# Kernel optimization log

Hardware: AMD Instinct MI355X
Metric: run time of the kernel (lower is better)

Reference implementation:

```python
import jax, jax.numpy as jnp
import numpy as np

EMB, HID, OUT = 512, 512, 512

def setup_inputs() -> dict:
    key = jax.random.key(0)
    ks = jax.random.split(key, 7)
    s = 1.0 / np.sqrt(EMB + HID)
    so = 1.0 / np.sqrt(2 * HID)
    return {
        "input_seq": jax.random.normal(ks[0], (32, 512, EMB), dtype=jnp.float32),
        "W_f": jax.random.uniform(ks[1], (EMB + HID, HID), jnp.float32, -s, s),
        "b_f": jax.random.uniform(ks[2], (HID,), jnp.float32, -s, s),
        "W_b": jax.random.uniform(ks[3], (EMB + HID, HID), jnp.float32, -s, s),
        "b_b": jax.random.uniform(ks[4], (HID,), jnp.float32, -s, s),
        "W_o": jax.random.uniform(ks[5], (2 * HID, OUT), jnp.float32, -so, so),
        "b_o": jax.random.uniform(ks[6], (OUT,), jnp.float32, -so, so),
    }

def _rnn_scan(xs, W, b, h0, reverse):
    # split W into input and hidden parts to avoid per-step concat
    Wx, Wh = W[:EMB], W[EMB:]
    def step(h, x_t):
        h_new = jnp.tanh(x_t @ Wx + h @ Wh + b)
        return h_new, h_new
    _, hs = jax.lax.scan(step, h0, xs, reverse=reverse)  # hs: [S, B, H]
    return hs

def reference(input_seq, W_f, b_f, W_b, b_b, W_o, b_o):
    B = input_seq.shape[0]
    xs = jnp.swapaxes(input_seq, 0, 1)  # [S, B, E]
    h0 = jnp.zeros((B, HID), input_seq.dtype)
    hs_f = _rnn_scan(xs, W_f, b_f, h0, reverse=False)   # [S, B, H]
    hs_b = _rnn_scan(xs, W_b, b_b, h0, reverse=True)    # [S, B, H], already time-aligned
    bi = jnp.concatenate([hs_f, hs_b], axis=-1)          # [S, B, 2H]
    out = bi @ W_o + b_o                                 # [S, B, O]
    return jnp.swapaxes(out, 0, 1)                       # [B, S, O]
```

## Files before the change

### kernel.cpp

```cpp
#include <hip/hip_runtime.h>
#include <hip/hip_fp16.h>
#include <stdint.h>

#define SEQ 512
#define HIDN 512

typedef _Float16 h2_t __attribute__((ext_vector_type(2)));
typedef _Float16 h8_t __attribute__((ext_vector_type(8)));
typedef float f4_t __attribute__((ext_vector_type(4)));

__device__ __forceinline__ float fdot2f(uint32_t a, uint32_t b, float c) {
#if __has_builtin(__builtin_amdgcn_fdot2)
  return __builtin_amdgcn_fdot2(__builtin_bit_cast(h2_t, a),
                                __builtin_bit_cast(h2_t, b), c, false);
#else
  h2_t ah = __builtin_bit_cast(h2_t, a);
  h2_t bh = __builtin_bit_cast(h2_t, b);
  return c + (float)ah.x * (float)bh.x + (float)ah.y * (float)bh.y;
#endif
}

__global__ void k_cvt(const float4* __restrict__ src, __half2* __restrict__ dst, int n4) {
  int i = blockIdx.x * blockDim.x + threadIdx.x;
  if (i < n4) {
    float4 v = src[i];
    dst[2 * i]     = __floats2half2_rn(v.x, v.y);
    dst[2 * i + 1] = __floats2half2_rn(v.z, v.w);
  }
}

__global__ void k_transpose_cvt(const float* __restrict__ src, __half* __restrict__ dst,
                                int R, int C) {
  __shared__ float tile[32][33];
  int tx = threadIdx.x, ty = threadIdx.y;
  int c0 = blockIdx.x * 32, r0 = blockIdx.y * 32;
#pragma unroll
  for (int i = 0; i < 4; ++i)
    tile[ty + i * 8][tx] = src[(size_t)(r0 + ty + i * 8) * C + c0 + tx];
  __syncthreads();
#pragma unroll
  for (int i = 0; i < 4; ++i)
    dst[(size_t)(c0 + ty + i * 8) * R + r0 + tx] = __float2half(tile[tx][ty + i * 8]);
}

__global__ __launch_bounds__(256, 2) void k_gemm(
    const __half* __restrict__ A, const __half* __restrict__ Bt,
    const float* __restrict__ bias, float* __restrict__ C,
    int M, int N, int K) {
  __shared__ __align__(16) __half As[128 * 32];
  __shared__ __align__(16) __half Bs[128 * 32];
  const int tid = threadIdx.x;
  const int m0 = blockIdx.x * 128;
  const int n0 = blockIdx.y * 128;
  const int w = tid >> 6;
  const int lane = tid & 63;
  const int wm = (w >> 1) * 64;
  const int wn = (w & 1) * 64;
  const int fr = lane & 15;
  const int q = lane >> 4;
  const int lr = tid >> 2;
  const int lc = tid & 3;
  f4_t acc[4][4];
#pragma unroll
  for (int i = 0; i < 4; ++i)
#pragma unroll
    for (int jj = 0; jj < 4; ++jj) acc[i][jj] = (f4_t)(0.f);

  for (int kk = 0; kk < K; kk += 32) {
    *(uint4*)&As[lr * 32 + lc * 8]        = *(const uint4*)&A[(size_t)(m0 + lr) * K + kk + lc * 8];
    *(uint4*)&As[(64 + lr) * 32 + lc * 8] = *(const uint4*)&A[(size_t)(m0 + 64 + lr) * K + kk + lc * 8];
    *(uint4*)&Bs[lr * 32 + lc * 8]        = *(const uint4*)&Bt[(size_t)(n0 + lr) * K + kk + lc * 8];
    *(uint4*)&Bs[(64 + lr) * 32 + lc * 8] = *(const uint4*)&Bt[(size_t)(n0 + 64 + lr) * K + kk + lc * 8];
    __syncthreads();
    h8_t af[4], bf[4];
#pragma unroll
    for (int i = 0; i < 4; ++i) {
      af[i] = *(const h8_t*)&As[(wm + i * 16 + fr) * 32 + q * 8];
      bf[i] = *(const h8_t*)&Bs[(wn + i * 16 + fr) * 32 + q * 8];
    }
#pragma unroll
    for (int i = 0; i < 4; ++i)
#pragma unroll
      for (int jj = 0; jj < 4; ++jj)
        acc[i][jj] = __builtin_amdgcn_mfma_f32_16x16x32_f16(af[i], bf[jj], acc[i][jj], 0, 0, 0);
    __syncthreads();
  }
#pragma unroll
  for (int i = 0; i < 4; ++i) {
    const int row0 = m0 + wm + i * 16 + q * 4;
#pragma unroll
    for (int jj = 0; jj < 4; ++jj) {
      const int col = n0 + wn + jj * 16 + fr;
      const float bv = bias[col];
#pragma unroll
      for (int r = 0; r < 4; ++r)
        C[(size_t)(row0 + r) * N + col] = acc[i][jj][r] + bv;
    }
  }
}

__global__ __launch_bounds__(1024) void k_rnn(
    const __half* __restrict__ WhT_f, const __half* __restrict__ WhT_b,
    const float* __restrict__ A_f, const float* __restrict__ A_b,
    __half* __restrict__ bi) {
  __shared__ __align__(16) uint4 ldsw4[9 * 1024];
  __shared__ __align__(16) __half hbuf[2][HIDN];
  __shared__ float psum[2][HIDN];
  const int t = threadIdx.x;
  const int j = t & 511;
  const int half = t >> 9;
  const int d = blockIdx.x & 1;
  const int b = blockIdx.x >> 1;
  const __half* WhT = d ? WhT_b : WhT_f;
  const float* A = (d ? A_b : A_f) + (size_t)b * SEQ * HIDN;
  __half* birow = bi + (size_t)b * SEQ * 1024 + d * HIDN + j;

  const uint4* wrow4 = (const uint4*)(WhT + (size_t)j * HIDN);
  uint4 wv[23];
#pragma unroll
  for (int i = 0; i < 23; ++i) wv[i] = wrow4[half * 32 + i];
#pragma unroll
  for (int p = 0; p < 9; ++p) ldsw4[p * 1024 + t] = wrow4[half * 32 + 23 + p];
  if (half == 0) hbuf[0][j] = __float2half(0.f);
  __syncthreads();

  const int tstep = d ? -1 : 1;
  int tt = d ? (SEQ - 1) : 0;
  float a_next = A[(size_t)tt * HIDN + j];
  int cur = 0;
  for (int s = 0; s < SEQ; ++s) {
    float a_cur = a_next;
    int tn = tt + tstep;
    tn = tn < 0 ? 0 : (tn > SEQ - 1 ? SEQ - 1 : tn);
    a_next = A[(size_t)tn * HIDN + j];
    const uint4* hp = (const uint4*)hbuf[cur] + half * 32;
    float acc0 = 0.f, acc1 = 0.f, acc2 = 0.f, acc3 = 0.f;
#pragma unroll
    for (int i = 0; i < 23; ++i) {
      uint4 hv = hp[i];
      acc0 = fdot2f(hv.x, wv[i].x, acc0);
      acc1 = fdot2f(hv.y, wv[i].y, acc1);
      acc2 = fdot2f(hv.z, wv[i].z, acc2);
      acc3 = fdot2f(hv.w, wv[i].w, acc3);
    }
#pragma unroll
    for (int p = 0; p < 9; ++p) {
      uint4 hv = hp[23 + p];
      uint4 lw = ldsw4[p * 1024 + t];
      acc0 = fdot2f(hv.x, lw.x, acc0);
      acc1 = fdot2f(hv.y, lw.y, acc1);
      acc2 = fdot2f(hv.z, lw.z, acc2);
      acc3 = fdot2f(hv.w, lw.w, acc3);
    }
    psum[half][j] = (acc0 + acc1) + (acc2 + acc3);
    __syncthreads();
    float p = psum[0][j] + psum[1][j] + a_cur;
    float ap = fabsf(p);
    float e = __expf(2.f * ap);
    float th = 1.f - 2.f * __builtin_amdgcn_rcpf(e + 1.f);
    float h = copysignf(th, p);
    __half hh = __float2half(h);
    hbuf[cur ^ 1][j] = hh;
    if (half == 0) birow[(size_t)tt * 1024] = hh;
    cur ^= 1;
    tt += tstep;
    __syncthreads();
  }
}

extern "C" void kernel_launch(void* const* d_in, const int* in_sizes, int n_in,
                              void* d_out, int out_size, void* d_ws, size_t ws_size,
                              hipStream_t stream) {
  const float* input_seq = (const float*)d_in[0];
  const float* W_f = (const float*)d_in[1];
  const float* b_f = (const float*)d_in[2];
  const float* W_b = (const float*)d_in[3];
  const float* b_b = (const float*)d_in[4];
  const float* W_o = (const float*)d_in[5];
  const float* b_o = (const float*)d_in[6];
  float* out = (float*)d_out;

  char* ws = (char*)d_ws;
  __half* Xh    = (__half*)(ws);
  float*  A_f   = (float*)(ws + 16777216);
  float*  A_b   = (float*)(ws + 50331648);
  __half* bi    = (__half*)(ws + 83886080);
  __half* WxT_f = (__half*)(ws + 117440512);
  __half* WxT_b = (__half*)(ws + 117964800);
  __half* WhT_f = (__half*)(ws + 118489088);
  __half* WhT_b = (__half*)(ws + 119013376);
  __half* WoT   = (__half*)(ws + 119537664);

  k_cvt<<<8192, 256, 0, stream>>>((const float4*)input_seq, (__half2*)Xh, 2097152);
  dim3 tb(32, 8);
  k_transpose_cvt<<<dim3(16, 16), tb, 0, stream>>>(W_f,          WxT_f, 512, 512);
  k_transpose_cvt<<<dim3(16, 16), tb, 0, stream>>>(W_f + 262144, WhT_f, 512, 512);
  k_transpose_cvt<<<dim3(16, 16), tb, 0, stream>>>(W_b,          WxT_b, 512, 512);
  k_transpose_cvt<<<dim3(16, 16), tb, 0, stream>>>(W_b + 262144, WhT_b, 512, 512);
  k_transpose_cvt<<<dim3(16, 32), tb, 0, stream>>>(W_o,          WoT, 1024, 512);

  k_gemm<<<dim3(128, 4), 256, 0, stream>>>(Xh, WxT_f, b_f, A_f, 16384, 512, 512);
  k_gemm<<<dim3(128, 4), 256, 0, stream>>>(Xh, WxT_b, b_b, A_b, 16384, 512, 512);

  k_rnn<<<64, 1024, 0, stream>>>(WhT_f, WhT_b, A_f, A_b, bi);

  k_gemm<<<dim3(128, 4), 256, 0, stream>>>(bi, WoT, b_o, out, 16384, 512, 1024);
}
```

Before: 998.5 us.

## Repartition RNN recurrence into 4-column by K-slice tiles with prepacked weights

Adds a packing kernel that rearranges the recurrent weight matrix so each thread reads coalesced uint4 chunks covering four output columns over a 64-element K slice. The RNN kernel now splits work across 8 K-slices and reduces partial sums through shared memory. Most weights are re-read from global memory (expected to hit cache) each step instead of being held in registers, with only 5 chunks kept in LDS. This aims to cut register pressure and the h-vector LDS reads, but it adds per-step global traffic and a wider 8-way reduction on the serial critical path.

New measurement: 2.083 ms. 109% more time.

```diff
diff --git a/kernel.cpp b/kernel.cpp
--- a/kernel.cpp
+++ b/kernel.cpp
@@ -41,6 +41,16 @@
 #pragma unroll
   for (int i = 0; i < 4; ++i)
     dst[(size_t)(c0 + ty + i * 8) * R + r0 + tx] = __float2half(tile[tx][ty + i * 8]);
+}
+
+__global__ void k_pack(const __half* __restrict__ WhT_f, const __half* __restrict__ WhT_b,
+                       uint4* __restrict__ Wp_f, uint4* __restrict__ Wp_b) {
+  int gid = blockIdx.x * blockDim.x + threadIdx.x;
+  int d = gid >> 15, r = gid & 32767, m = r >> 10, t = r & 1023;
+  int cg = t & 127, ks = t >> 7, col = cg * 4 + (m >> 3), sub = m & 7;
+  const __half* W = d ? WhT_b : WhT_f;
+  uint4 v = ((const uint4*)(W + (size_t)col * HIDN))[ks * 8 + sub];
+  (d ? Wp_b : Wp_f)[m * 1024 + t] = v;
 }
 
 __global__ __launch_bounds__(256, 2) void k_gemm(
@@ -100,68 +110,67 @@
 }
 
 __global__ __launch_bounds__(1024) void k_rnn(
-    const __half* __restrict__ WhT_f, const __half* __restrict__ WhT_b,
+    const uint4* __restrict__ Wp_f, const uint4* __restrict__ Wp_b,
     const float* __restrict__ A_f, const float* __restrict__ A_b,
     __half* __restrict__ bi) {
-  __shared__ __align__(16) uint4 ldsw4[9 * 1024];
+  __shared__ __align__(16) uint4 ldsw4[5 * 1024];
   __shared__ __align__(16) __half hbuf[2][HIDN];
-  __shared__ float psum[2][HIDN];
+  __shared__ __align__(16) float psum[8 * HIDN];
   const int t = threadIdx.x;
-  const int j = t & 511;
-  const int half = t >> 9;
+  const int ks = t >> 7;
+  const int cg = t & 127;
   const int d = blockIdx.x & 1;
   const int b = blockIdx.x >> 1;
-  const __half* WhT = d ? WhT_b : WhT_f;
+  const uint4* Wp = d ? Wp_b : Wp_f;
   const float* A = (d ? A_b : A_f) + (size_t)b * SEQ * HIDN;
-  __half* birow = bi + (size_t)b * SEQ * 1024 + d * HIDN + j;
-
-  const uint4* wrow4 = (const uint4*)(WhT + (size_t)j * HIDN);
-  uint4 wv[23];
-#pragma unroll
-  for (int i = 0; i < 23; ++i) wv[i] = wrow4[half * 32 + i];
-#pragma unroll
-  for (int p = 0; p < 9; ++p) ldsw4[p * 1024 + t] = wrow4[half * 32 + 23 + p];
-  if (half == 0) hbuf[0][j] = __float2half(0.f);
+
+#pragma unroll
+  for (int m = 0; m < 5; ++m) ldsw4[m * 1024 + t] = Wp[m * 1024 + t];
+  if (t < HIDN) hbuf[0][t] = __float2half(0.f);
   __syncthreads();
+
+  const char* wp = (const char*)Wp;
 
   const int tstep = d ? -1 : 1;
   int tt = d ? (SEQ - 1) : 0;
-  float a_next = A[(size_t)tt * HIDN + j];
+  float a_next = (t < HIDN) ? A[(size_t)tt * HIDN + t] : 0.f;
   int cur = 0;
   for (int s = 0; s < SEQ; ++s) {
-    float a_cur = a_next;
-    int tn = tt + tstep;
-    tn = tn < 0 ? 0 : (tn > SEQ - 1 ? SEQ - 1 : tn);
-    a_next = A[(size_t)tn * HIDN + j];
-    const uint4* hp = (const uint4*)hbuf[cur] + half * 32;
-    float acc0 = 0.f, acc1 = 0.f, acc2 = 0.f, acc3 = 0.f;
-#pragma unroll
-    for (int i = 0; i < 23; ++i) {
-      uint4 hv = hp[i];
-      acc0 = fdot2f(hv.x, wv[i].x, acc0);
-      acc1 = fdot2f(hv.y, wv[i].y, acc1);
-      acc2 = fdot2f(hv.z, wv[i].z, acc2);
-      acc3 = fdot2f(hv.w, wv[i].w, acc3);
-    }
-#pragma unroll
-    for (int p = 0; p < 9; ++p) {
-      uint4 hv = hp[23 + p];
-      uint4 lw = ldsw4[p * 1024 + t];
-      acc0 = fdot2f(hv.x, lw.x, acc0);
-      acc1 = fdot2f(hv.y, lw.y, acc1);
-      acc2 = fdot2f(hv.z, lw.z, acc2);
-      acc3 = fdot2f(hv.w, lw.w, acc3);
-    }
-    psum[half][j] = (acc0 + acc1) + (acc2 + acc3);
-    __syncthreads();
-    float p = psum[0][j] + psum[1][j] + a_cur;
-    float ap = fabsf(p);
-    float e = __expf(2.f * ap);
-    float th = 1.f - 2.f * __builtin_amdgcn_rcpf(e + 1.f);
-    float h = copysignf(th, p);
-    __half hh = __float2half(h);
-    hbuf[cur ^ 1][j] = hh;
-    if (half == 0) birow[(size_t)tt * 1024] = hh;
+    asm volatile("" : "+s"(wp));
+    const uint4* hp = (const uint4*)hbuf[cur] + (ks << 3);
+    uint4 hv[8];
+#pragma unroll
+    for (int u = 0; u < 8; ++u) hv[u] = hp[u];
+    float acc[4] = {0.f, 0.f, 0.f, 0.f};
+#pragma unroll
+    for (int m = 0; m < 32; ++m) {
+      const int ci = m >> 3, sub = m & 7;
+      uint4 w;
+      if (m < 5) w = ldsw4[m * 1024 + t];
+      else       w = *(const uint4*)(wp + (((size_t)m * 1024 + t) << 4));
+      acc[ci] = fdot2f(hv[sub].x, w.x, acc[ci]);
+      acc[ci] = fdot2f(hv[sub].y, w.y, acc[ci]);
+      acc[ci] = fdot2f(hv[sub].z, w.z, acc[ci]);
+      acc[ci] = fdot2f(hv[sub].w, w.w, acc[ci]);
+    }
+    *(f4_t*)&psum[ks * HIDN + cg * 4] = (f4_t){acc[0], acc[1], acc[2], acc[3]};
+    __syncthreads();
+    if (t < HIDN) {
+      float a_cur = a_next;
+      float p = a_cur +
+          ((psum[t] + psum[HIDN + t]) + (psum[2 * HIDN + t] + psum[3 * HIDN + t])) +
+          ((psum[4 * HIDN + t] + psum[5 * HIDN + t]) + (psum[6 * HIDN + t] + psum[7 * HIDN + t]));
+      float ap = fabsf(p);
+      float e = __expf(2.f * ap);
+      float th = 1.f - 2.f * __builtin_amdgcn_rcpf(e + 1.f);
+      float h = copysignf(th, p);
+      __half hh = __float2half(h);
+      hbuf[cur ^ 1][t] = hh;
+      bi[(size_t)b * SEQ * 1024 + (size_t)tt * 1024 + d * HIDN + t] = hh;
+      int tn = tt + tstep;
+      tn = tn < 0 ? 0 : (tn > SEQ - 1 ? SEQ - 1 : tn);
+      a_next = A[(size_t)tn * HIDN + t];
+    }
     cur ^= 1;
     tt += tstep;
     __syncthreads();
@@ -190,6 +199,8 @@
   __half* WhT_f = (__half*)(ws + 118489088);
   __half* WhT_b = (__half*)(ws + 119013376);
   __half* WoT   = (__half*)(ws + 119537664);
+  uint4*  Wp_f  = (uint4*)(ws + 120586240);
+  uint4*  Wp_b  = (uint4*)(ws + 121110528);
 
   k_cvt<<<8192, 256, 0, stream>>>((const float4*)input_seq, (__half2*)Xh, 2097152);
   dim3 tb(32, 8);
@@ -198,11 +209,12 @@
   k_transpose_cvt<<<dim3(16, 16), tb, 0, stream>>>(W_b,          WxT_b, 512, 512);
   k_transpose_cvt<<<dim3(16, 16), tb, 0, stream>>>(W_b + 262144, WhT_b, 512, 512);
   k_transpose_cvt<<<dim3(16, 32), tb, 0, stream>>>(W_o,          WoT, 1024, 512);
+  k_pack<<<256, 256, 0, stream>>>(WhT_f, WhT_b, Wp_f, Wp_b);
 
   k_gemm<<<dim3(128, 4), 256, 0, stream>>>(Xh, WxT_f, b_f, A_f, 16384, 512, 512);
   k_gemm<<<dim3(128, 4), 256, 0, stream>>>(Xh, WxT_b, b_b, A_b, 16384, 512, 512);
 
-  k_rnn<<<64, 1024, 0, stream>>>(WhT_f, WhT_b, A_f, A_b, bi);
+  k_rnn<<<64, 1024, 0, stream>>>(Wp_f, Wp_b, A_f, A_b, bi);
 
   k_gemm<<<dim3(128, 4), 256, 0, stream>>>(bi, WoT, b_o, out, 16384, 512, 1024);
 }
```

## Split each RNN chain across four blocks with global-memory flag synchronization

Applied to the files above, without the earlier changes.

Each recurrent chain (batch, direction) is now spread over four workgroups, each owning 128 hidden columns, so 256 blocks run instead of 64. All recurrent weights now fit in LDS, and each thread's serial dot-product work per step shrinks. Hidden states are exchanged through a global double buffer, with per-step release/acquire flag spinning between the four blocks of a chain. This adds cross-block latency on every step and relies on all 256 blocks being co-resident; the block-to-XCD mapping is chosen to keep a chain's blocks on the same XCD.

Result: slower. 3.504 ms (+251.0%).

```diff
diff --git a/kernel.cpp b/kernel.cpp
--- a/kernel.cpp
+++ b/kernel.cpp
@@ -4,6 +4,7 @@
 
 #define SEQ 512
 #define HIDN 512
+#define CHAINS 64
 
 typedef _Float16 h2_t __attribute__((ext_vector_type(2)));
 typedef _Float16 h8_t __attribute__((ext_vector_type(8)));
@@ -102,67 +103,75 @@
 __global__ __launch_bounds__(1024) void k_rnn(
     const __half* __restrict__ WhT_f, const __half* __restrict__ WhT_b,
     const float* __restrict__ A_f, const float* __restrict__ A_b,
-    __half* __restrict__ bi) {
-  __shared__ __align__(16) uint4 ldsw4[9 * 1024];
-  __shared__ __align__(16) __half hbuf[2][HIDN];
-  __shared__ float psum[2][HIDN];
+    __half* __restrict__ bi, __half* __restrict__ Hx,
+    unsigned int* __restrict__ flags) {
+  __shared__ __align__(16) uint4 w4[8192];
+  __shared__ __align__(16) __half hbuf[HIDN];
+  __shared__ float psum[1024];
   const int t = threadIdx.x;
-  const int j = t & 511;
-  const int half = t >> 9;
-  const int d = blockIdx.x & 1;
-  const int b = blockIdx.x >> 1;
+  const int B = blockIdx.x;
+  const int xcd = B & 7, q = B >> 3;
+  const int part = q & 3, slot = q >> 2;
+  const int c = slot * 8 + xcd;
+  const int d = c & 1, b = c >> 1;
+  const int c0 = part * 128;
   const __half* WhT = d ? WhT_b : WhT_f;
   const float* A = (d ? A_b : A_f) + (size_t)b * SEQ * HIDN;
-  __half* birow = bi + (size_t)b * SEQ * 1024 + d * HIDN + j;
-
-  const uint4* wrow4 = (const uint4*)(WhT + (size_t)j * HIDN);
-  uint4 wv[23];
-#pragma unroll
-  for (int i = 0; i < 23; ++i) wv[i] = wrow4[half * 32 + i];
-#pragma unroll
-  for (int p = 0; p < 9; ++p) ldsw4[p * 1024 + t] = wrow4[half * 32 + 23 + p];
-  if (half == 0) hbuf[0][j] = __float2half(0.f);
+  const int col = t & 127, ks = t >> 7;
+
+  {
+    const uint4* wr = (const uint4*)(WhT + (size_t)(c0 + col) * HIDN);
+#pragma unroll
+    for (int u = 0; u < 8; ++u) w4[(ks * 8 + u) * 128 + col] = wr[ks * 8 + u];
+  }
+  if (t < HIDN) hbuf[t] = __float2half(0.f);
   __syncthreads();
 
+  unsigned int* myflags = flags + c * 4;
   const int tstep = d ? -1 : 1;
   int tt = d ? (SEQ - 1) : 0;
-  float a_next = A[(size_t)tt * HIDN + j];
-  int cur = 0;
+  float a_next = (t < 128) ? A[(size_t)tt * HIDN + c0 + t] : 0.f;
+
   for (int s = 0; s < SEQ; ++s) {
-    float a_cur = a_next;
-    int tn = tt + tstep;
-    tn = tn < 0 ? 0 : (tn > SEQ - 1 ? SEQ - 1 : tn);
-    a_next = A[(size_t)tn * HIDN + j];
-    const uint4* hp = (const uint4*)hbuf[cur] + half * 32;
-    float acc0 = 0.f, acc1 = 0.f, acc2 = 0.f, acc3 = 0.f;
-#pragma unroll
-    for (int i = 0; i < 23; ++i) {
-      uint4 hv = hp[i];
-      acc0 = fdot2f(hv.x, wv[i].x, acc0);
-      acc1 = fdot2f(hv.y, wv[i].y, acc1);
-      acc2 = fdot2f(hv.z, wv[i].z, acc2);
-      acc3 = fdot2f(hv.w, wv[i].w, acc3);
-    }
-#pragma unroll
-    for (int p = 0; p < 9; ++p) {
-      uint4 hv = hp[23 + p];
-      uint4 lw = ldsw4[p * 1024 + t];
-      acc0 = fdot2f(hv.x, lw.x, acc0);
-      acc1 = fdot2f(hv.y, lw.y, acc1);
-      acc2 = fdot2f(hv.z, lw.z, acc2);
-      acc3 = fdot2f(hv.w, lw.w, acc3);
-    }
-    psum[half][j] = (acc0 + acc1) + (acc2 + acc3);
-    __syncthreads();
-    float p = psum[0][j] + psum[1][j] + a_cur;
-    float ap = fabsf(p);
-    float e = __expf(2.f * ap);
-    float th = 1.f - 2.f * __builtin_amdgcn_rcpf(e + 1.f);
-    float h = copysignf(th, p);
-    __half hh = __float2half(h);
-    hbuf[cur ^ 1][j] = hh;
-    if (half == 0) birow[(size_t)tt * 1024] = hh;
-    cur ^= 1;
+    const uint4* hp = (const uint4*)hbuf + ks * 8;
+    float ac0 = 0.f, ac1 = 0.f, ac2 = 0.f, ac3 = 0.f;
+#pragma unroll
+    for (int u = 0; u < 8; ++u) {
+      uint4 hv = hp[u];
+      uint4 w = w4[(ks * 8 + u) * 128 + col];
+      ac0 = fdot2f(hv.x, w.x, ac0);
+      ac1 = fdot2f(hv.y, w.y, ac1);
+      ac2 = fdot2f(hv.z, w.z, ac2);
+      ac3 = fdot2f(hv.w, w.w, ac3);
+    }
+    psum[ks * 128 + col] = (ac0 + ac1) + (ac2 + ac3);
+    __syncthreads();
+    __half* HxS = Hx + ((size_t)(s & 1) * CHAINS + c) * HIDN;
+    if (t < 128) {
+      float p = a_next;
+#pragma unroll
+      for (int u = 0; u < 8; ++u) p += psum[u * 128 + t];
+      float ap = fabsf(p);
+      float e = __expf(2.f * ap);
+      float th = 1.f - 2.f * __builtin_amdgcn_rcpf(e + 1.f);
+      float h = copysignf(th, p);
+      __half hh = __float2half(h);
+      HxS[c0 + t] = hh;
+      bi[(size_t)b * SEQ * 1024 + (size_t)tt * 1024 + d * HIDN + c0 + t] = hh;
+      int tn = tt + tstep;
+      tn = tn < 0 ? 0 : (tn > SEQ - 1 ? SEQ - 1 : tn);
+      a_next = A[(size_t)tn * HIDN + c0 + t];
+    }
+    __syncthreads();
+    if (t == 0)
+      __hip_atomic_store(&myflags[part], (unsigned int)(s + 1),
+                         __ATOMIC_RELEASE, __HIP_MEMORY_SCOPE_AGENT);
+    if (t < 4) {
+      while (__hip_atomic_load(&myflags[t], __ATOMIC_ACQUIRE,
+                               __HIP_MEMORY_SCOPE_AGENT) <= (unsigned int)s) {}
+    }
+    __syncthreads();
+    if (t < 256) ((unsigned int*)hbuf)[t] = ((const unsigned int*)HxS)[t];
     tt += tstep;
     __syncthreads();
   }
@@ -190,6 +199,10 @@
   __half* WhT_f = (__half*)(ws + 118489088);
   __half* WhT_b = (__half*)(ws + 119013376);
   __half* WoT   = (__half*)(ws + 119537664);
+  __half* Hx    = (__half*)(ws + 120586240);
+  unsigned int* flags = (unsigned int*)(ws + 120717312);
+
+  hipMemsetAsync(flags, 0, CHAINS * 4 * sizeof(unsigned int), stream);
 
   k_cvt<<<8192, 256, 0, stream>>>((const float4*)input_seq, (__half2*)Xh, 2097152);
   dim3 tb(32, 8);
@@ -202,7 +215,7 @@
   k_gemm<<<dim3(128, 4), 256, 0, stream>>>(Xh, WxT_f, b_f, A_f, 16384, 512, 512);
   k_gemm<<<dim3(128, 4), 256, 0, stream>>>(Xh, WxT_b, b_b, A_b, 16384, 512, 512);
 
-  k_rnn<<<64, 1024, 0, stream>>>(WhT_f, WhT_b, A_f, A_b, bi);
+  k_rnn<<<256, 1024, 0, stream>>>(WhT_f, WhT_b, A_f, A_b, bi, Hx, flags);
 
   k_gemm<<<dim3(128, 4), 256, 0, stream>>>(bi, WoT, b_o, out, 16384, 512, 1024);
 }
```
